# Performance work log

Measured on AMD Instinct MI355X. Metric: run time of the kernel, lower is better.

Reference implementation:

```python
import jax, jax.numpy as jnp
import numpy as np

B, S, D, H = 2, 2048, 1024, 16
DK = D // H

def setup_inputs() -> dict:
    key = jax.random.key(0)
    ks = jax.random.split(key, 11)
    scale = 1.0 / np.sqrt(D)
    inp = {
        'q': jax.random.normal(ks[0], (B, S, D), jnp.float32),
        'k': jax.random.normal(ks[1], (B, S, D), jnp.float32),
        'v': jax.random.normal(ks[2], (B, S, D), jnp.float32),
        'Wq': jax.random.normal(ks[3], (D, D), jnp.float32) * scale,
        'bq': jnp.zeros((D,), jnp.float32),
        'Wk': jax.random.normal(ks[4], (D, D), jnp.float32) * scale,
        'bk': jnp.zeros((D,), jnp.float32),
        'Wv': jax.random.normal(ks[5], (D, D), jnp.float32) * scale,
        'bv': jnp.zeros((D,), jnp.float32),
        'Wo': jax.random.normal(ks[6], (D, D), jnp.float32) * scale,
        'bo': jnp.zeros((D,), jnp.float32),
    }
    return inp

def reference(q, k, v, Wq, bq, Wk, bk, Wv, bv, Wo, bo):
    # linear projections
    qp = q @ Wq + bq   # [B,S,D]
    kp = k @ Wk + bk
    vp = v @ Wv + bv
    # split heads -> [B,H,S,DK]
    qh = qp.reshape(B, S, H, DK).transpose(0, 2, 1, 3)
    kh = kp.reshape(B, S, H, DK).transpose(0, 2, 1, 3)
    vh = vp.reshape(B, S, H, DK).transpose(0, 2, 1, 3)
    scaled = jnp.einsum('bhqd,bhkd->bhqk', qh, kh) / jnp.sqrt(jnp.float32(DK))
    attn_score = jax.nn.softmax(scaled, axis=-1)  # [B,H,S,S]
    x = jnp.einsum('bhqk,bhkd->bhqd', attn_score, vh)
    # dropout is identity in eval mode
    out = x.transpose(0, 2, 1, 3).reshape(B, S, D)
    return (out @ Wo + bo, attn_score)
```

## Files before the change

### kernel.cpp

```cpp
#include <hip/hip_runtime.h>
#include <hip/hip_bf16.h>
#include <stdint.h>
#include <stddef.h>

typedef unsigned short u16;
typedef __attribute__((ext_vector_type(8))) short short8;
typedef __attribute__((ext_vector_type(4))) short bfx4;
typedef __attribute__((ext_vector_type(4))) float f32x4;
typedef __attribute__((ext_vector_type(4))) float f4;

constexpr int B_ = 2, S_ = 2048, D_ = 1024, H_ = 16;
constexpr size_t OUT_ELEMS = (size_t)B_ * S_ * D_;

__device__ __forceinline__ u16 f2bf(float f) {
    union { float f; unsigned u; } v; v.f = f;
    unsigned r = 0x7FFFu + ((v.u >> 16) & 1u);
    return (u16)((v.u + r) >> 16);
}

__device__ __forceinline__ unsigned cvtpk(float lo, float hi) {
    unsigned r;
    asm("v_cvt_pk_bf16_f32 %0, %1, %2" : "=v"(r) : "v"(lo), "v"(hi));
    return r;
}

__device__ __forceinline__ void gload16(const void* g, void* l) {
    auto gg = reinterpret_cast<const __attribute__((address_space(1))) unsigned*>(
        reinterpret_cast<uintptr_t>(g));
    auto ll = reinterpret_cast<__attribute__((address_space(3))) unsigned*>(
        reinterpret_cast<uintptr_t>(l));
    __builtin_amdgcn_global_load_lds(gg, ll, 16, 0, 0);
}

#define VMWAIT(N) do { asm volatile("s_waitcnt vmcnt(" #N ")" ::: "memory"); } while (0)
#define LGKMWAIT0() do { asm volatile("s_waitcnt lgkmcnt(0)" ::: "memory"); } while (0)
__device__ __forceinline__ void barrier_() {
    __builtin_amdgcn_s_barrier();
    __builtin_amdgcn_sched_barrier(0);
}

__global__ __launch_bounds__(256) void wtrans_kernel(
    const float* __restrict__ W0, const float* __restrict__ W1,
    const float* __restrict__ W2, const float* __restrict__ W3,
    u16* __restrict__ T0, u16* __restrict__ T1, u16* __restrict__ T2, u16* __restrict__ T3)
{
    __shared__ __align__(16) u16 Ts[64][72];
    const float* W = blockIdx.z == 0 ? W0 : blockIdx.z == 1 ? W1 : blockIdx.z == 2 ? W2 : W3;
    u16*         T = blockIdx.z == 0 ? T0 : blockIdx.z == 1 ? T1 : blockIdx.z == 2 ? T2 : T3;
    const int t = threadIdx.x;
    const int r0 = blockIdx.y * 64, c0 = blockIdx.x * 64;
    const int row = t >> 2, qd = t & 3;

    const float* src = W + (size_t)(r0 + row) * 1024 + c0 + qd * 16;
    u16 tmp[16];
    #pragma unroll
    for (int j = 0; j < 16; j += 4) {
        f4 v = *(const f4*)(src + j);
        tmp[j] = f2bf(v[0]); tmp[j+1] = f2bf(v[1]); tmp[j+2] = f2bf(v[2]); tmp[j+3] = f2bf(v[3]);
    }
    #pragma unroll
    for (int j = 0; j < 16; j++) Ts[row][qd * 16 + j] = tmp[j];
    __syncthreads();
    short8 o0, o1;
    #pragma unroll
    for (int j = 0; j < 8; j++) { o0[j] = (short)Ts[qd*16 + j][row]; o1[j] = (short)Ts[qd*16 + 8 + j][row]; }
    u16* dst = T + (size_t)(c0 + row) * 1024 + r0 + qd * 16;
    *(short8*)dst = o0;
    *(short8*)(dst + 8) = o1;
}

__global__ __launch_bounds__(256) void vtrans_kernel(const u16* __restrict__ vp, u16* __restrict__ vt)
{
    __shared__ __align__(16) u16 Vs[64][72];
    const int t = threadIdx.x;
    const int s0 = blockIdx.x * 64;
    const int bh = blockIdx.y, b = bh >> 4, h = bh & 15;
    #pragma unroll
    for (int i = 0; i < 2; i++) {
        int c = t + 256 * i, row = c >> 3, ch = c & 7;
        *(short8*)(&Vs[row][ch * 8]) =
            *(const short8*)(vp + ((size_t)b * S_ + s0 + row) * D_ + h * 64 + ch * 8);
    }
    __syncthreads();
    #pragma unroll
    for (int i = 0; i < 2; i++) {
        int c = t + 256 * i, d = c >> 3, ch = c & 7;
        short8 o;
        #pragma unroll
        for (int j = 0; j < 8; j++) o[j] = (short)Vs[ch * 8 + j][d];
        *(short8*)(vt + ((size_t)bh * 64 + d) * S_ + s0 + ch * 8) = o;
    }
}

struct StageF { f4 v[4]; };

__device__ __forceinline__ void a_load(StageF& st, const float* Af, int row0, int k0, int t) {
    const int row = t >> 1, half = t & 1;
    const float* p = Af + (size_t)(row0 + row) * D_ + k0 + half * 16;
    st.v[0] = *(const f4*)(p);
    st.v[1] = *(const f4*)(p + 4);
    st.v[2] = *(const f4*)(p + 8);
    st.v[3] = *(const f4*)(p + 12);
}

__device__ __forceinline__ void a_store(const StageF& st, u16* Ls, int t) {
    const int row = t >> 1, half = t & 1;
    union { unsigned u[4]; short8 s8; } h0, h1;
    h0.u[0] = cvtpk(st.v[0][0], st.v[0][1]); h0.u[1] = cvtpk(st.v[0][2], st.v[0][3]);
    h0.u[2] = cvtpk(st.v[1][0], st.v[1][1]); h0.u[3] = cvtpk(st.v[1][2], st.v[1][3]);
    h1.u[0] = cvtpk(st.v[2][0], st.v[2][1]); h1.u[1] = cvtpk(st.v[2][2], st.v[2][3]);
    h1.u[2] = cvtpk(st.v[3][0], st.v[3][1]); h1.u[3] = cvtpk(st.v[3][2], st.v[3][3]);
    const int sw = (row & 3) << 4;
    *(short8*)((char*)Ls + row * 64 + ((half * 32) ^ sw))      = h0.s8;
    *(short8*)((char*)Ls + row * 64 + ((half * 32 + 16) ^ sw)) = h1.s8;
}

__global__ __launch_bounds__(256, 3)
void gemm_qkvf(const float* __restrict__ A0, const float* __restrict__ A1, const float* __restrict__ A2,
               const u16* __restrict__ Bt0, const u16* __restrict__ Bt1, const u16* __restrict__ Bt2,
               const float* __restrict__ bi0, const float* __restrict__ bi1, const float* __restrict__ bi2,
               u16* __restrict__ Cq, u16* __restrict__ Ck, u16* __restrict__ Cv)
{
    constexpr int K = D_, N = D_;
    __shared__ __align__(16) u16 As[2][128 * 32];
    __shared__ __align__(16) u16 Bs[2][128 * 32];

    const int z = blockIdx.z;
    const float* Aptr = z == 0 ? A0  : z == 1 ? A1  : A2;
    const u16*   Bt   = z == 0 ? Bt0 : z == 1 ? Bt1 : Bt2;
    const float* bias = z == 0 ? bi0 : z == 1 ? bi1 : bi2;
    u16*         Cptr = z == 0 ? Cq  : z == 1 ? Ck  : Cv;
    const float scale = z == 0 ? 0.125f : 1.0f;

    const int t = threadIdx.x;
    const int w = t >> 6, l = t & 63, lr = l >> 4, lc = l & 15;
    const int wr = w >> 1, wc = w & 1;
    const int id = blockIdx.y * 8 + blockIdx.x;
    const int xcd = id & 7, i_ = id >> 3;
    const int row0 = ((xcd << 2) | ((i_ >> 4) << 1) | ((i_ >> 3) & 1)) * 128;
    const int col0 = (i_ & 7) * 128;
    const int NI = K >> 5;

    auto issueB = [&](int i, u16* dst) {
        #pragma unroll
        for (int j = 0; j < 2; j++) {
            int off = j * 256 + t;
            int row = off >> 2, ch = off & 3;
            const char* src = (const char*)Bt + (((size_t)(col0 + row) * K + i * 32) << 1)
                              + ((ch ^ (row & 3)) << 4);
            gload16(src, (char*)dst + off * 16);
        }
    };

    f32x4 acc[4][4] = {};
    StageF sa;
    issueB(0, Bs[0]);
    a_load(sa, Aptr, row0, 0, t);

    for (int i = 0; i < NI; i++) {
        const int p = i & 1;
        a_store(sa, As[p], t);
        LGKMWAIT0();
        barrier_();
        if (i + 1 < NI) {
            issueB(i + 1, Bs[p ^ 1]);
            a_load(sa, Aptr, row0, (i + 1) * 32, t);
        }

        short8 af[4], bf_[4];
        #pragma unroll
        for (int mm = 0; mm < 4; mm++) {
            int r = wr * 64 + mm * 16 + lc;
            af[mm] = *(const short8*)((const char*)As[p] + r * 64 + ((lr * 16) ^ ((r & 3) << 4)));
        }
        #pragma unroll
        for (int nn = 0; nn < 4; nn++) {
            int r = wc * 64 + nn * 16 + lc;
            bf_[nn] = *(const short8*)((const char*)Bs[p] + r * 64 + ((lr * 16) ^ ((r & 3) << 4)));
        }
        #pragma unroll
        for (int mm = 0; mm < 4; mm++)
            #pragma unroll
            for (int nn = 0; nn < 4; nn++)
                acc[mm][nn] = __builtin_amdgcn_mfma_f32_16x16x32_bf16(af[mm], bf_[nn], acc[mm][nn], 0, 0, 0);
    }

    float bv[4];
    #pragma unroll
    for (int nn = 0; nn < 4; nn++) bv[nn] = bias[col0 + wc * 64 + nn * 16 + lc];

    #pragma unroll
    for (int mm = 0; mm < 4; mm++) {
        const int row = row0 + wr * 64 + mm * 16 + lr * 4;
        #pragma unroll
        for (int nn = 0; nn < 4; nn++) {
            const int col = col0 + wc * 64 + nn * 16 + lc;
            #pragma unroll
            for (int r = 0; r < 4; r++)
                Cptr[(size_t)(row + r) * N + col] = f2bf((acc[mm][nn][r] + bv[nn]) * scale);
        }
    }
}

__global__ __launch_bounds__(256, 3)
void gemm_out(const u16* __restrict__ Aptr, const u16* __restrict__ Bt,
              const float* __restrict__ bias, float* __restrict__ Cptr)
{
    constexpr int K = D_, N = D_;
    __shared__ __align__(16) u16 As[2][128 * 32];
    __shared__ __align__(16) u16 Bs[2][128 * 32];

    const int t = threadIdx.x;
    const int w = t >> 6, l = t & 63, lr = l >> 4, lc = l & 15;
    const int wr = w >> 1, wc = w & 1;
    const int id = blockIdx.y * 8 + blockIdx.x;
    const int xcd = id & 7, i_ = id >> 3;
    const int row0 = ((xcd << 2) | ((i_ >> 4) << 1) | ((i_ >> 3) & 1)) * 128;
    const int col0 = (i_ & 7) * 128;
    const int NI = K >> 5;

    auto issueT = [&](const u16* P, int r0_, int i, u16* dst) {
        #pragma unroll
        for (int j = 0; j < 2; j++) {
            int off = j * 256 + t;
            int row = off >> 2, ch = off & 3;
            const char* src = (const char*)P + (((size_t)(r0_ + row) * K + i * 32) << 1)
                              + ((ch ^ (row & 3)) << 4);
            gload16(src, (char*)dst + off * 16);
        }
    };

    f32x4 acc[4][4] = {};
    issueT(Bt, col0, 0, Bs[0]);
    issueT(Aptr, row0, 0, As[0]);

    for (int i = 0; i < NI; i++) {
        const int p = i & 1;
        if (i + 1 < NI) {
            issueT(Bt, col0, i + 1, Bs[p ^ 1]);
            issueT(Aptr, row0, i + 1, As[p ^ 1]);
            VMWAIT(4);
        } else {
            VMWAIT(0);
        }
        barrier_();

        short8 af[4], bf_[4];
        #pragma unroll
        for (int mm = 0; mm < 4; mm++) {
            int r = wr * 64 + mm * 16 + lc;
            af[mm] = *(const short8*)((const char*)As[p] + r * 64 + ((lr * 16) ^ ((r & 3) << 4)));
        }
        #pragma unroll
        for (int nn = 0; nn < 4; nn++) {
            int r = wc * 64 + nn * 16 + lc;
            bf_[nn] = *(const short8*)((const char*)Bs[p] + r * 64 + ((lr * 16) ^ ((r & 3) << 4)));
        }
        #pragma unroll
        for (int mm = 0; mm < 4; mm++)
            #pragma unroll
            for (int nn = 0; nn < 4; nn++)
                acc[mm][nn] = __builtin_amdgcn_mfma_f32_16x16x32_bf16(af[mm], bf_[nn], acc[mm][nn], 0, 0, 0);
        __builtin_amdgcn_s_barrier();
    }

    float bv[4];
    #pragma unroll
    for (int nn = 0; nn < 4; nn++) bv[nn] = bias[col0 + wc * 64 + nn * 16 + lc];

    #pragma unroll
    for (int mm = 0; mm < 4; mm++) {
        const int row = row0 + wr * 64 + mm * 16 + lr * 4;
        #pragma unroll
        for (int nn = 0; nn < 4; nn++) {
            const int col = col0 + wc * 64 + nn * 16 + lc;
            #pragma unroll
            for (int r = 0; r < 4; r++)
                Cptr[(size_t)(row + r) * N + col] = acc[mm][nn][r] + bv[nn];
        }
    }
}

__global__ __launch_bounds__(512, 4)
void attn_kernel(const u16* __restrict__ qp, const u16* __restrict__ kp,
                 const u16* __restrict__ vt, float* __restrict__ Pout,
                 u16* __restrict__ xout)
{
    __shared__ __align__(16) u16 Qs[128 * 64];
    __shared__ __align__(16) u16 Ks[2][128 * 64];
    __shared__ __align__(16) u16 Vts[2][64 * 128];

    const int t = threadIdx.x;
    const int w = t >> 6, l = t & 63, lr = l >> 4, lc = l & 15;
    const int bid = blockIdx.x;
    const int s = ((bid & 7) << 6) | (bid >> 3);
    const int q0 = (s & 15) * 128;
    const int bh = s >> 4, b = bh >> 4, h = bh & 15;
    const float L2E = 1.4426950408889634f;
    constexpr int NT = S_ / 128;

    auto issueK = [&](int kt, int buf) {
        #pragma unroll
        for (int i = 0; i < 2; i++) {
            int off = i * 512 + t, row = off >> 3, ch = off & 7;
            const char* src = (const char*)kp + ((((size_t)b * S_ + kt * 128 + row) * D_ + h * 64) << 1)
                              + ((ch ^ (row & 7)) << 4);
            gload16(src, (char*)Ks[buf] + off * 16);
        }
    };
    auto issueV = [&](int kt, int buf) {
        #pragma unroll
        for (int i = 0; i < 2; i++) {
            int off = i * 512 + t, row = off >> 4, ch = off & 15;
            const char* src = (const char*)vt + ((((size_t)bh * 64 + row) * S_ + kt * 128) << 1)
                              + ((ch ^ (row & 7)) << 4);
            gload16(src, (char*)Vts[buf] + off * 16);
        }
    };

    issueK(0, 0);
    #pragma unroll
    for (int i = 0; i < 2; i++) {
        int c = t + 512 * i, row = c >> 3, ch = c & 7;
        short8 vq = *(const short8*)(qp + ((size_t)b * S_ + q0 + row) * D_ + h * 64 + ch * 8);
        *(short8*)((char*)Qs + row * 128 + ((ch * 16) ^ ((row & 7) << 4))) = vq;
    }
    __syncthreads();

    short8 qf[2];
    {
        int r = w * 16 + lc, sw = (r & 7) << 4;
        const char* qb = (const char*)Qs + r * 128;
        qf[0] = *(const short8*)(qb + ((lr * 16) ^ sw));
        qf[1] = *(const short8*)(qb + ((64 + lr * 16) ^ sw));
    }

    float sum = 0.f;
    for (int kt = 0; kt < NT; kt++) {
        const int p = kt & 1;
        if (kt + 1 < NT) { issueK(kt + 1, p ^ 1); VMWAIT(2); }
        else             { VMWAIT(0); }
        barrier_();
        const char* Kb = (const char*)Ks[p];
        #pragma unroll
        for (int f = 0; f < 8; f++) {
            int r = f * 16 + lc, sw = (r & 7) << 4;
            const char* kb = Kb + r * 128;
            short8 k0 = *(const short8*)(kb + ((lr * 16) ^ sw));
            short8 k1 = *(const short8*)(kb + ((64 + lr * 16) ^ sw));
            f32x4 sacc = {};
            sacc = __builtin_amdgcn_mfma_f32_16x16x32_bf16(k0, qf[0], sacc, 0, 0, 0);
            sacc = __builtin_amdgcn_mfma_f32_16x16x32_bf16(k1, qf[1], sacc, 0, 0, 0);
            sum += exp2f(sacc[0] * L2E) + exp2f(sacc[1] * L2E)
                 + exp2f(sacc[2] * L2E) + exp2f(sacc[3] * L2E);
        }
        __builtin_amdgcn_s_barrier();
    }
    issueK(0, 0); issueV(0, 0);
    sum += __shfl_xor(sum, 16);
    sum += __shfl_xor(sum, 32);
    const float inv = 1.0f / sum;

    f32x4 xacc[4] = {};
    float* pbase = Pout + ((size_t)bh * S_ + q0 + w * 16 + lc) * S_ + lr * 4;

    for (int kt = 0; kt < NT; kt++) {
        const int p = kt & 1;
        if (kt + 1 < NT) { issueK(kt + 1, p ^ 1); issueV(kt + 1, p ^ 1); }
        if (kt == 0)           VMWAIT(4);
        else if (kt + 1 < NT)  VMWAIT(12);
        else                   VMWAIT(8);
        barrier_();
        const char* Kb = (const char*)Ks[p];
        const char* Vb = (const char*)Vts[p];

        #pragma unroll
        for (int kk = 0; kk < 4; kk++) {
            union { unsigned u[4]; short8 s8; } pu;
            #pragma unroll
            for (int fo = 0; fo < 2; fo++) {
                const int f = kk * 2 + fo;
                int r = f * 16 + lc, sw = (r & 7) << 4;
                const char* kb = Kb + r * 128;
                short8 k0 = *(const short8*)(kb + ((lr * 16) ^ sw));
                short8 k1 = *(const short8*)(kb + ((64 + lr * 16) ^ sw));
                f32x4 sacc = {};
                __builtin_amdgcn_s_setprio(1);
                sacc = __builtin_amdgcn_mfma_f32_16x16x32_bf16(k0, qf[0], sacc, 0, 0, 0);
                sacc = __builtin_amdgcn_mfma_f32_16x16x32_bf16(k1, qf[1], sacc, 0, 0, 0);
                __builtin_amdgcn_s_setprio(0);
                f32x4 pv_;
                pv_[0] = exp2f(sacc[0] * L2E) * inv;
                pv_[1] = exp2f(sacc[1] * L2E) * inv;
                pv_[2] = exp2f(sacc[2] * L2E) * inv;
                pv_[3] = exp2f(sacc[3] * L2E) * inv;
                *(f32x4*)(pbase + (size_t)kt * 128 + f * 16) = pv_;
                pu.u[fo * 2 + 0] = cvtpk(pv_[0], pv_[1]);
                pu.u[fo * 2 + 1] = cvtpk(pv_[2], pv_[3]);
            }
            const short8 pa = pu.s8;
            __builtin_amdgcn_s_setprio(1);
            #pragma unroll
            for (int n = 0; n < 4; n++) {
                int rr = n * 16 + lc, sw2 = (rr & 7) << 4;
                const char* vrow = Vb + rr * 256;
                union { bfx4 h[2]; short8 s8; } vu;
                vu.h[0] = *(const bfx4*)(vrow + ((kk * 64 + lr * 8) ^ sw2));
                vu.h[1] = *(const bfx4*)(vrow + ((kk * 64 + 32 + lr * 8) ^ sw2));
                xacc[n] = __builtin_amdgcn_mfma_f32_16x16x32_bf16(pa, vu.s8, xacc[n], 0, 0, 0);
            }
            __builtin_amdgcn_s_setprio(0);
        }
        __builtin_amdgcn_s_barrier();
    }

    #pragma unroll
    for (int n = 0; n < 4; n++) {
        #pragma unroll
        for (int r = 0; r < 4; r++) {
            int row = q0 + w * 16 + lr * 4 + r;
            int col = h * 64 + n * 16 + lc;
            xout[((size_t)b * S_ + row) * D_ + col] = f2bf(xacc[n][r]);
        }
    }
}

extern "C" void kernel_launch(void* const* d_in, const int* in_sizes, int n_in,
                              void* d_out, int out_size, void* d_ws, size_t ws_size,
                              hipStream_t stream)
{
    const float* qin = (const float*)d_in[0];
    const float* kin = (const float*)d_in[1];
    const float* vin = (const float*)d_in[2];
    const float* Wq  = (const float*)d_in[3];
    const float* bq  = (const float*)d_in[4];
    const float* Wk  = (const float*)d_in[5];
    const float* bk  = (const float*)d_in[6];
    const float* Wv  = (const float*)d_in[7];
    const float* bv  = (const float*)d_in[8];
    const float* Wo  = (const float*)d_in[9];
    const float* bo  = (const float*)d_in[10];

    u16* base = (u16*)d_ws;
    u16* Wqt = base;
    u16* Wkt = base + 1048576;
    u16* Wvt = base + 2097152;
    u16* Wot = base + 3145728;
    u16* qpb = base + 4194304;
    u16* kpb = base + 8388608;
    u16* vpb = base + 12582912;
    u16* vtb = base + 16777216;
    u16* xb  = base + 20971520;

    float* out  = (float*)d_out;
    float* Pout = out + OUT_ELEMS;

    wtrans_kernel<<<dim3(16, 16, 4), 256, 0, stream>>>(Wq, Wk, Wv, Wo, Wqt, Wkt, Wvt, Wot);
    gemm_qkvf<<<dim3(8, 32, 3), 256, 0, stream>>>(
        qin, kin, vin, Wqt, Wkt, Wvt, bq, bk, bv, qpb, kpb, vpb);
    vtrans_kernel<<<dim3(32, 32), 256, 0, stream>>>(vpb, vtb);
    attn_kernel<<<512, 512, 0, stream>>>(qpb, kpb, vtb, Pout, xb);
    gemm_out<<<dim3(8, 32), 256, 0, stream>>>(xb, Wot, bo, out);
}
```

Baseline: 274.9 us.

## Give each attention wave two query sub-tiles and halve block threads

The attention kernel now runs 256 threads per block, and each wave handles 32 query rows as two 16-row sub-tiles. Each K and V fragment read from LDS is therefore reused for twice as many MFMAs. Q fragments are loaded straight from global memory into registers, dropping the Q shared-memory stage and its sync. Softmax normalisation folds -log2(sum) into the exponent via fma instead of a separate multiply. Register pressure rises, and each thread issues more global loads per tile, so occupancy may fall.

```diff
diff --git a/kernel.cpp b/kernel.cpp
--- a/kernel.cpp
+++ b/kernel.cpp
@@ -281,12 +281,11 @@
     }
 }
 
-__global__ __launch_bounds__(512, 4)
+__global__ __launch_bounds__(256, 2)
 void attn_kernel(const u16* __restrict__ qp, const u16* __restrict__ kp,
                  const u16* __restrict__ vt, float* __restrict__ Pout,
                  u16* __restrict__ xout)
 {
-    __shared__ __align__(16) u16 Qs[128 * 64];
     __shared__ __align__(16) u16 Ks[2][128 * 64];
     __shared__ __align__(16) u16 Vts[2][64 * 128];
 
@@ -301,8 +300,8 @@
 
     auto issueK = [&](int kt, int buf) {
         #pragma unroll
-        for (int i = 0; i < 2; i++) {
-            int off = i * 512 + t, row = off >> 3, ch = off & 7;
+        for (int i = 0; i < 4; i++) {
+            int off = i * 256 + t, row = off >> 3, ch = off & 7;
             const char* src = (const char*)kp + ((((size_t)b * S_ + kt * 128 + row) * D_ + h * 64) << 1)
                               + ((ch ^ (row & 7)) << 4);
             gload16(src, (char*)Ks[buf] + off * 16);
@@ -310,8 +309,8 @@
     };
     auto issueV = [&](int kt, int buf) {
         #pragma unroll
-        for (int i = 0; i < 2; i++) {
-            int off = i * 512 + t, row = off >> 4, ch = off & 15;
+        for (int i = 0; i < 4; i++) {
+            int off = i * 256 + t, row = off >> 4, ch = off & 15;
             const char* src = (const char*)vt + ((((size_t)bh * 64 + row) * S_ + kt * 128) << 1)
                               + ((ch ^ (row & 7)) << 4);
             gload16(src, (char*)Vts[buf] + off * 16);
@@ -319,26 +318,18 @@
     };
 
     issueK(0, 0);
-    #pragma unroll
-    for (int i = 0; i < 2; i++) {
-        int c = t + 512 * i, row = c >> 3, ch = c & 7;
-        short8 vq = *(const short8*)(qp + ((size_t)b * S_ + q0 + row) * D_ + h * 64 + ch * 8);
-        *(short8*)((char*)Qs + row * 128 + ((ch * 16) ^ ((row & 7) << 4))) = vq;
-    }
-    __syncthreads();
-
-    short8 qf[2];
-    {
-        int r = w * 16 + lc, sw = (r & 7) << 4;
-        const char* qb = (const char*)Qs + r * 128;
-        qf[0] = *(const short8*)(qb + ((lr * 16) ^ sw));
-        qf[1] = *(const short8*)(qb + ((64 + lr * 16) ^ sw));
-    }
-
-    float sum = 0.f;
+    short8 qf[2][2];
+    #pragma unroll
+    for (int qh = 0; qh < 2; qh++) {
+        const u16* qrow = qp + ((size_t)b * S_ + q0 + w * 32 + qh * 16 + lc) * D_ + h * 64;
+        qf[qh][0] = *(const short8*)(qrow + lr * 8);
+        qf[qh][1] = *(const short8*)(qrow + 32 + lr * 8);
+    }
+
+    float sum0 = 0.f, sum1 = 0.f;
     for (int kt = 0; kt < NT; kt++) {
         const int p = kt & 1;
-        if (kt + 1 < NT) { issueK(kt + 1, p ^ 1); VMWAIT(2); }
+        if (kt + 1 < NT) { issueK(kt + 1, p ^ 1); VMWAIT(4); }
         else             { VMWAIT(0); }
         barrier_();
         const char* Kb = (const char*)Ks[p];
@@ -348,35 +339,41 @@
             const char* kb = Kb + r * 128;
             short8 k0 = *(const short8*)(kb + ((lr * 16) ^ sw));
             short8 k1 = *(const short8*)(kb + ((64 + lr * 16) ^ sw));
-            f32x4 sacc = {};
-            sacc = __builtin_amdgcn_mfma_f32_16x16x32_bf16(k0, qf[0], sacc, 0, 0, 0);
-            sacc = __builtin_amdgcn_mfma_f32_16x16x32_bf16(k1, qf[1], sacc, 0, 0, 0);
-            sum += exp2f(sacc[0] * L2E) + exp2f(sacc[1] * L2E)
-                 + exp2f(sacc[2] * L2E) + exp2f(sacc[3] * L2E);
+            f32x4 s0 = {}, s1 = {};
+            s0 = __builtin_amdgcn_mfma_f32_16x16x32_bf16(k0, qf[0][0], s0, 0, 0, 0);
+            s0 = __builtin_amdgcn_mfma_f32_16x16x32_bf16(k1, qf[0][1], s0, 0, 0, 0);
+            s1 = __builtin_amdgcn_mfma_f32_16x16x32_bf16(k0, qf[1][0], s1, 0, 0, 0);
+            s1 = __builtin_amdgcn_mfma_f32_16x16x32_bf16(k1, qf[1][1], s1, 0, 0, 0);
+            sum0 += exp2f(s0[0] * L2E) + exp2f(s0[1] * L2E)
+                  + exp2f(s0[2] * L2E) + exp2f(s0[3] * L2E);
+            sum1 += exp2f(s1[0] * L2E) + exp2f(s1[1] * L2E)
+                  + exp2f(s1[2] * L2E) + exp2f(s1[3] * L2E);
         }
         __builtin_amdgcn_s_barrier();
     }
     issueK(0, 0); issueV(0, 0);
-    sum += __shfl_xor(sum, 16);
-    sum += __shfl_xor(sum, 32);
-    const float inv = 1.0f / sum;
-
-    f32x4 xacc[4] = {};
-    float* pbase = Pout + ((size_t)bh * S_ + q0 + w * 16 + lc) * S_ + lr * 4;
+    sum0 += __shfl_xor(sum0, 16); sum0 += __shfl_xor(sum0, 32);
+    sum1 += __shfl_xor(sum1, 16); sum1 += __shfl_xor(sum1, 32);
+    const float l2i0 = -log2f(sum0);
+    const float l2i1 = -log2f(sum1);
+
+    f32x4 xacc[2][4] = {};
+    float* pb0 = Pout + ((size_t)bh * S_ + q0 + w * 32 + lc) * S_ + lr * 4;
+    float* pb1 = pb0 + (size_t)16 * S_;
 
     for (int kt = 0; kt < NT; kt++) {
         const int p = kt & 1;
         if (kt + 1 < NT) { issueK(kt + 1, p ^ 1); issueV(kt + 1, p ^ 1); }
-        if (kt == 0)           VMWAIT(4);
-        else if (kt + 1 < NT)  VMWAIT(12);
-        else                   VMWAIT(8);
+        if (kt == 0)           VMWAIT(8);
+        else if (kt + 1 < NT)  VMWAIT(24);
+        else                   VMWAIT(16);
         barrier_();
         const char* Kb = (const char*)Ks[p];
         const char* Vb = (const char*)Vts[p];
 
         #pragma unroll
         for (int kk = 0; kk < 4; kk++) {
-            union { unsigned u[4]; short8 s8; } pu;
+            union { unsigned u[4]; short8 s8; } pu0, pu1;
             #pragma unroll
             for (int fo = 0; fo < 2; fo++) {
                 const int f = kk * 2 + fo;
@@ -384,21 +381,26 @@
                 const char* kb = Kb + r * 128;
                 short8 k0 = *(const short8*)(kb + ((lr * 16) ^ sw));
                 short8 k1 = *(const short8*)(kb + ((64 + lr * 16) ^ sw));
-                f32x4 sacc = {};
+                f32x4 s0 = {}, s1 = {};
                 __builtin_amdgcn_s_setprio(1);
-                sacc = __builtin_amdgcn_mfma_f32_16x16x32_bf16(k0, qf[0], sacc, 0, 0, 0);
-                sacc = __builtin_amdgcn_mfma_f32_16x16x32_bf16(k1, qf[1], sacc, 0, 0, 0);
+                s0 = __builtin_amdgcn_mfma_f32_16x16x32_bf16(k0, qf[0][0], s0, 0, 0, 0);
+                s0 = __builtin_amdgcn_mfma_f32_16x16x32_bf16(k1, qf[0][1], s0, 0, 0, 0);
+                s1 = __builtin_amdgcn_mfma_f32_16x16x32_bf16(k0, qf[1][0], s1, 0, 0, 0);
+                s1 = __builtin_amdgcn_mfma_f32_16x16x32_bf16(k1, qf[1][1], s1, 0, 0, 0);
                 __builtin_amdgcn_s_setprio(0);
-                f32x4 pv_;
-                pv_[0] = exp2f(sacc[0] * L2E) * inv;
-                pv_[1] = exp2f(sacc[1] * L2E) * inv;
-                pv_[2] = exp2f(sacc[2] * L2E) * inv;
-                pv_[3] = exp2f(sacc[3] * L2E) * inv;
-                *(f32x4*)(pbase + (size_t)kt * 128 + f * 16) = pv_;
-                pu.u[fo * 2 + 0] = cvtpk(pv_[0], pv_[1]);
-                pu.u[fo * 2 + 1] = cvtpk(pv_[2], pv_[3]);
+                f32x4 p0, p1;
+                p0[0] = exp2f(fmaf(s0[0], L2E, l2i0)); p0[1] = exp2f(fmaf(s0[1], L2E, l2i0));
+                p0[2] = exp2f(fmaf(s0[2], L2E, l2i0)); p0[3] = exp2f(fmaf(s0[3], L2E, l2i0));
+                p1[0] = exp2f(fmaf(s1[0], L2E, l2i1)); p1[1] = exp2f(fmaf(s1[1], L2E, l2i1));
+                p1[2] = exp2f(fmaf(s1[2], L2E, l2i1)); p1[3] = exp2f(fmaf(s1[3], L2E, l2i1));
+                *(f32x4*)(pb0 + (size_t)kt * 128 + f * 16) = p0;
+                *(f32x4*)(pb1 + (size_t)kt * 128 + f * 16) = p1;
+                pu0.u[fo * 2 + 0] = cvtpk(p0[0], p0[1]);
+                pu0.u[fo * 2 + 1] = cvtpk(p0[2], p0[3]);
+                pu1.u[fo * 2 + 0] = cvtpk(p1[0], p1[1]);
+                pu1.u[fo * 2 + 1] = cvtpk(p1[2], p1[3]);
             }
-            const short8 pa = pu.s8;
+            const short8 pa0 = pu0.s8, pa1 = pu1.s8;
             __builtin_amdgcn_s_setprio(1);
             #pragma unroll
             for (int n = 0; n < 4; n++) {
@@ -407,7 +409,8 @@
                 union { bfx4 h[2]; short8 s8; } vu;
                 vu.h[0] = *(const bfx4*)(vrow + ((kk * 64 + lr * 8) ^ sw2));
                 vu.h[1] = *(const bfx4*)(vrow + ((kk * 64 + 32 + lr * 8) ^ sw2));
-                xacc[n] = __builtin_amdgcn_mfma_f32_16x16x32_bf16(pa, vu.s8, xacc[n], 0, 0, 0);
+                xacc[0][n] = __builtin_amdgcn_mfma_f32_16x16x32_bf16(pa0, vu.s8, xacc[0][n], 0, 0, 0);
+                xacc[1][n] = __builtin_amdgcn_mfma_f32_16x16x32_bf16(pa1, vu.s8, xacc[1][n], 0, 0, 0);
             }
             __builtin_amdgcn_s_setprio(0);
         }
@@ -415,12 +418,15 @@
     }
 
     #pragma unroll
-    for (int n = 0; n < 4; n++) {
-        #pragma unroll
-        for (int r = 0; r < 4; r++) {
-            int row = q0 + w * 16 + lr * 4 + r;
-            int col = h * 64 + n * 16 + lc;
-            xout[((size_t)b * S_ + row) * D_ + col] = f2bf(xacc[n][r]);
+    for (int qh = 0; qh < 2; qh++) {
+        #pragma unroll
+        for (int n = 0; n < 4; n++) {
+            #pragma unroll
+            for (int r = 0; r < 4; r++) {
+                int row = q0 + w * 32 + qh * 16 + lr * 4 + r;
+                int col = h * 64 + n * 16 + lc;
+                xout[((size_t)b * S_ + row) * D_ + col] = f2bf(xacc[qh][n][r]);
+            }
         }
     }
 }
@@ -459,6 +465,6 @@
     gemm_qkvf<<<dim3(8, 32, 3), 256, 0, stream>>>(
         qin, kin, vin, Wqt, Wkt, Wvt, bq, bk, bv, qpb, kpb, vpb);
     vtrans_kernel<<<dim3(32, 32), 256, 0, stream>>>(vpb, vtb);
-    attn_kernel<<<512, 512, 0, stream>>>(qpb, kpb, vtb, Pout, xb);
+    attn_kernel<<<512, 256, 0, stream>>>(qpb, kpb, vtb, Pout, xb);
     gemm_out<<<dim3(8, 32), 256, 0, stream>>>(xb, Wot, bo, out);
 }
```

Measured after the change: 290.6 us. 5.7% more time.

## Split softmax row-sum pass into separate high-parallelism kernel

Applied to the files above, without the earlier changes.

The first pass of the attention kernel, which computes softmax denominators over all key tiles, is moved into a new rowsum kernel launched with 8192 blocks. Each block handles one query tile and one key tile and writes partial sums to a workspace buffer. The attention kernel then adds up the 16 partials, drops the Q shared-memory staging, and folds the normalization into the exponent as exp2(s*L2E - log2(sum)). This spreads the denominator pass over far more parallelism than 512 blocks allow, at the cost of an extra launch, a second read of K, and a partial-sum buffer round trip.

```diff
diff --git a/kernel.cpp b/kernel.cpp
--- a/kernel.cpp
+++ b/kernel.cpp
@@ -281,12 +281,64 @@
     }
 }
 
+__global__ __launch_bounds__(256)
+void rowsum_kernel(const u16* __restrict__ qp, const u16* __restrict__ kp,
+                   float* __restrict__ partial)
+{
+    __shared__ __align__(16) u16 Ks[128 * 64];
+
+    const int t = threadIdx.x;
+    const int w = t >> 6, l = t & 63, lr = l >> 4, lc = l & 15;
+    const int bid = blockIdx.x;
+    const int s = ((bid & 7) << 10) | (bid >> 3);
+    const int kt = s & 15, qt = (s >> 4) & 15, bh = s >> 8;
+    const int b = bh >> 4, h = bh & 15;
+    const float L2E = 1.4426950408889634f;
+
+    #pragma unroll
+    for (int i = 0; i < 4; i++) {
+        int off = i * 256 + t, row = off >> 3, ch = off & 7;
+        const char* src = (const char*)kp + ((((size_t)b * S_ + kt * 128 + row) * D_ + h * 64) << 1)
+                          + ((ch ^ (row & 7)) << 4);
+        gload16(src, (char*)Ks + off * 16);
+    }
+    short8 qf[2][2];
+    #pragma unroll
+    for (int qh = 0; qh < 2; qh++) {
+        const u16* qrow = qp + ((size_t)b * S_ + qt * 128 + w * 32 + qh * 16 + lc) * D_ + h * 64;
+        qf[qh][0] = *(const short8*)(qrow + lr * 8);
+        qf[qh][1] = *(const short8*)(qrow + 32 + lr * 8);
+    }
+    __syncthreads();
+
+    float e0 = 0.f, e1 = 0.f;
+    #pragma unroll
+    for (int f = 0; f < 8; f++) {
+        int r = f * 16 + lc, sw = (r & 7) << 4;
+        const char* kb = (const char*)Ks + r * 128;
+        short8 k0 = *(const short8*)(kb + ((lr * 16) ^ sw));
+        short8 k1 = *(const short8*)(kb + ((64 + lr * 16) ^ sw));
+        f32x4 s0 = {}, s1 = {};
+        s0 = __builtin_amdgcn_mfma_f32_16x16x32_bf16(k0, qf[0][0], s0, 0, 0, 0);
+        s0 = __builtin_amdgcn_mfma_f32_16x16x32_bf16(k1, qf[0][1], s0, 0, 0, 0);
+        s1 = __builtin_amdgcn_mfma_f32_16x16x32_bf16(k0, qf[1][0], s1, 0, 0, 0);
+        s1 = __builtin_amdgcn_mfma_f32_16x16x32_bf16(k1, qf[1][1], s1, 0, 0, 0);
+        e0 += exp2f(s0[0] * L2E) + exp2f(s0[1] * L2E) + exp2f(s0[2] * L2E) + exp2f(s0[3] * L2E);
+        e1 += exp2f(s1[0] * L2E) + exp2f(s1[1] * L2E) + exp2f(s1[2] * L2E) + exp2f(s1[3] * L2E);
+    }
+    e0 += __shfl_xor(e0, 16); e0 += __shfl_xor(e0, 32);
+    e1 += __shfl_xor(e1, 16); e1 += __shfl_xor(e1, 32);
+    if (l < 32) {
+        float v = (l < 16) ? e0 : e1;
+        partial[((size_t)kt * 32 + bh) * 2048 + qt * 128 + w * 32 + l] = v;
+    }
+}
+
 __global__ __launch_bounds__(512, 4)
 void attn_kernel(const u16* __restrict__ qp, const u16* __restrict__ kp,
-                 const u16* __restrict__ vt, float* __restrict__ Pout,
-                 u16* __restrict__ xout)
-{
-    __shared__ __align__(16) u16 Qs[128 * 64];
+                 const u16* __restrict__ vt, const float* __restrict__ partial,
+                 float* __restrict__ Pout, u16* __restrict__ xout)
+{
     __shared__ __align__(16) u16 Ks[2][128 * 64];
     __shared__ __align__(16) u16 Vts[2][64 * 128];
 
@@ -318,48 +370,21 @@
         }
     };
 
-    issueK(0, 0);
-    #pragma unroll
-    for (int i = 0; i < 2; i++) {
-        int c = t + 512 * i, row = c >> 3, ch = c & 7;
-        short8 vq = *(const short8*)(qp + ((size_t)b * S_ + q0 + row) * D_ + h * 64 + ch * 8);
-        *(short8*)((char*)Qs + row * 128 + ((ch * 16) ^ ((row & 7) << 4))) = vq;
-    }
-    __syncthreads();
+    issueK(0, 0); issueV(0, 0);
 
     short8 qf[2];
     {
-        int r = w * 16 + lc, sw = (r & 7) << 4;
-        const char* qb = (const char*)Qs + r * 128;
-        qf[0] = *(const short8*)(qb + ((lr * 16) ^ sw));
-        qf[1] = *(const short8*)(qb + ((64 + lr * 16) ^ sw));
-    }
-
+        const u16* qrow = qp + ((size_t)b * S_ + q0 + w * 16 + lc) * D_ + h * 64;
+        qf[0] = *(const short8*)(qrow + lr * 8);
+        qf[1] = *(const short8*)(qrow + 32 + lr * 8);
+    }
     float sum = 0.f;
-    for (int kt = 0; kt < NT; kt++) {
-        const int p = kt & 1;
-        if (kt + 1 < NT) { issueK(kt + 1, p ^ 1); VMWAIT(2); }
-        else             { VMWAIT(0); }
-        barrier_();
-        const char* Kb = (const char*)Ks[p];
-        #pragma unroll
-        for (int f = 0; f < 8; f++) {
-            int r = f * 16 + lc, sw = (r & 7) << 4;
-            const char* kb = Kb + r * 128;
-            short8 k0 = *(const short8*)(kb + ((lr * 16) ^ sw));
-            short8 k1 = *(const short8*)(kb + ((64 + lr * 16) ^ sw));
-            f32x4 sacc = {};
-            sacc = __builtin_amdgcn_mfma_f32_16x16x32_bf16(k0, qf[0], sacc, 0, 0, 0);
-            sacc = __builtin_amdgcn_mfma_f32_16x16x32_bf16(k1, qf[1], sacc, 0, 0, 0);
-            sum += exp2f(sacc[0] * L2E) + exp2f(sacc[1] * L2E)
-                 + exp2f(sacc[2] * L2E) + exp2f(sacc[3] * L2E);
-        }
-        __builtin_amdgcn_s_barrier();
-    }
-    issueK(0, 0); issueV(0, 0);
-    sum += __shfl_xor(sum, 16);
-    sum += __shfl_xor(sum, 32);
-    const float inv = 1.0f / sum;
+    {
+        const float* pptr = partial + (size_t)bh * 2048 + q0 + w * 16 + lc;
+        #pragma unroll
+        for (int kt = 0; kt < 16; kt++) sum += pptr[(size_t)kt * 32 * 2048];
+    }
+    const float l2i = -log2f(sum);
 
     f32x4 xacc[4] = {};
     float* pbase = Pout + ((size_t)bh * S_ + q0 + w * 16 + lc) * S_ + lr * 4;
@@ -390,10 +415,10 @@
                 sacc = __builtin_amdgcn_mfma_f32_16x16x32_bf16(k1, qf[1], sacc, 0, 0, 0);
                 __builtin_amdgcn_s_setprio(0);
                 f32x4 pv_;
-                pv_[0] = exp2f(sacc[0] * L2E) * inv;
-                pv_[1] = exp2f(sacc[1] * L2E) * inv;
-                pv_[2] = exp2f(sacc[2] * L2E) * inv;
-                pv_[3] = exp2f(sacc[3] * L2E) * inv;
+                pv_[0] = exp2f(fmaf(sacc[0], L2E, l2i));
+                pv_[1] = exp2f(fmaf(sacc[1], L2E, l2i));
+                pv_[2] = exp2f(fmaf(sacc[2], L2E, l2i));
+                pv_[3] = exp2f(fmaf(sacc[3], L2E, l2i));
                 *(f32x4*)(pbase + (size_t)kt * 128 + f * 16) = pv_;
                 pu.u[fo * 2 + 0] = cvtpk(pv_[0], pv_[1]);
                 pu.u[fo * 2 + 1] = cvtpk(pv_[2], pv_[3]);
@@ -451,6 +476,7 @@
     u16* vpb = base + 12582912;
     u16* vtb = base + 16777216;
     u16* xb  = base + 20971520;
+    float* partial = (float*)(base + 25165824);
 
     float* out  = (float*)d_out;
     float* Pout = out + OUT_ELEMS;
@@ -459,6 +485,7 @@
     gemm_qkvf<<<dim3(8, 32, 3), 256, 0, stream>>>(
         qin, kin, vin, Wqt, Wkt, Wvt, bq, bk, bv, qpb, kpb, vpb);
     vtrans_kernel<<<dim3(32, 32), 256, 0, stream>>>(vpb, vtb);
-    attn_kernel<<<512, 512, 0, stream>>>(qpb, kpb, vtb, Pout, xb);
+    rowsum_kernel<<<8192, 256, 0, stream>>>(qpb, kpb, partial);
+    attn_kernel<<<512, 512, 0, stream>>>(qpb, kpb, vtb, partial, Pout, xb);
     gemm_out<<<dim3(8, 32), 256, 0, stream>>>(xb, Wot, bo, out);
 }
```

Result: slower. 287.4 us (+4.6%).

## Stage attention probabilities through LDS for coalesced row stores; fold normalization into exp

Applied to the files above, without the earlier changes.

Each wave now writes its 16x32 block of softmax probabilities into a per-wave swizzled LDS tile and reads it back so that eight lanes store 128 contiguous bytes per row of P. Previously each lane wrote 16-byte pieces spread across rows. The goal is better write coalescing for the large fp32 attention-score output. The division by the row sum is replaced by adding -log2(sum) inside the exp2 argument, and Q fragments are loaded straight from global memory instead of through LDS. The LDS round trip adds extra shared-memory traffic, and the row-to-lane mapping relies on wave-local ordering with no explicit sync.

```diff
diff --git a/kernel.cpp b/kernel.cpp
--- a/kernel.cpp
+++ b/kernel.cpp
@@ -286,9 +286,9 @@
                  const u16* __restrict__ vt, float* __restrict__ Pout,
                  u16* __restrict__ xout)
 {
-    __shared__ __align__(16) u16 Qs[128 * 64];
     __shared__ __align__(16) u16 Ks[2][128 * 64];
     __shared__ __align__(16) u16 Vts[2][64 * 128];
+    __shared__ __align__(16) float Pls[8][16][32];
 
     const int t = threadIdx.x;
     const int w = t >> 6, l = t & 63, lr = l >> 4, lc = l & 15;
@@ -319,20 +319,11 @@
     };
 
     issueK(0, 0);
-    #pragma unroll
-    for (int i = 0; i < 2; i++) {
-        int c = t + 512 * i, row = c >> 3, ch = c & 7;
-        short8 vq = *(const short8*)(qp + ((size_t)b * S_ + q0 + row) * D_ + h * 64 + ch * 8);
-        *(short8*)((char*)Qs + row * 128 + ((ch * 16) ^ ((row & 7) << 4))) = vq;
-    }
-    __syncthreads();
-
     short8 qf[2];
     {
-        int r = w * 16 + lc, sw = (r & 7) << 4;
-        const char* qb = (const char*)Qs + r * 128;
-        qf[0] = *(const short8*)(qb + ((lr * 16) ^ sw));
-        qf[1] = *(const short8*)(qb + ((64 + lr * 16) ^ sw));
+        const u16* qrow = qp + ((size_t)b * S_ + q0 + w * 16 + lc) * D_ + h * 64;
+        qf[0] = *(const short8*)(qrow + lr * 8);
+        qf[1] = *(const short8*)(qrow + 32 + lr * 8);
     }
 
     float sum = 0.f;
@@ -359,10 +350,11 @@
     issueK(0, 0); issueV(0, 0);
     sum += __shfl_xor(sum, 16);
     sum += __shfl_xor(sum, 32);
-    const float inv = 1.0f / sum;
+    const float l2i = -log2f(sum);
 
     f32x4 xacc[4] = {};
-    float* pbase = Pout + ((size_t)bh * S_ + q0 + w * 16 + lc) * S_ + lr * 4;
+    float* pls = &Pls[w][0][0];
+    float* prow0 = Pout + ((size_t)bh * S_ + q0 + w * 16) * S_;
 
     for (int kt = 0; kt < NT; kt++) {
         const int p = kt & 1;
@@ -390,13 +382,23 @@
                 sacc = __builtin_amdgcn_mfma_f32_16x16x32_bf16(k1, qf[1], sacc, 0, 0, 0);
                 __builtin_amdgcn_s_setprio(0);
                 f32x4 pv_;
-                pv_[0] = exp2f(sacc[0] * L2E) * inv;
-                pv_[1] = exp2f(sacc[1] * L2E) * inv;
-                pv_[2] = exp2f(sacc[2] * L2E) * inv;
-                pv_[3] = exp2f(sacc[3] * L2E) * inv;
-                *(f32x4*)(pbase + (size_t)kt * 128 + f * 16) = pv_;
+                pv_[0] = exp2f(fmaf(sacc[0], L2E, l2i));
+                pv_[1] = exp2f(fmaf(sacc[1], L2E, l2i));
+                pv_[2] = exp2f(fmaf(sacc[2], L2E, l2i));
+                pv_[3] = exp2f(fmaf(sacc[3], L2E, l2i));
+                *(f32x4*)((char*)pls + lc * 128 + (((fo * 64 + lr * 16)) ^ ((lc & 7) << 4))) = pv_;
                 pu.u[fo * 2 + 0] = cvtpk(pv_[0], pv_[1]);
                 pu.u[fo * 2 + 1] = cvtpk(pv_[2], pv_[3]);
+            }
+            {
+                float* prow = prow0 + (size_t)kt * 128 + kk * 32;
+                #pragma unroll
+                for (int half = 0; half < 2; half++) {
+                    int row = half * 8 + (l >> 3), chunk = l & 7;
+                    f32x4 pr = *(const f32x4*)((const char*)pls + row * 128
+                               + ((chunk * 16) ^ (((l >> 3) & 7) << 4)));
+                    *(f32x4*)(prow + (size_t)row * S_ + chunk * 4) = pr;
+                }
             }
             const short8 pa = pu.s8;
             __builtin_amdgcn_s_setprio(1);
```

Result: faster. 258.8 us, median of 2 (-5.8%).
